# Kernel tuning notes

Hardware: AMD Instinct MI355X
Metric: run time of the kernel (lower is better)

Reference implementation:

```python
import jax, jax.numpy as jnp
import numpy as np

S, B, HID = 2048, 1, 2048
NH, HD = 16, 128  # heads, head_dim (kv_channels); NH*HD == HID
EPS = 1e-5


def setup_inputs() -> dict:
    key = jax.random.key(0)
    ks = jax.random.split(key, 5)
    sc_h = 1.0 / np.sqrt(HID)
    return {
        "hidden_states": jax.random.normal(ks[0], (S, B, HID), jnp.float32),
        "ln_weight": jnp.ones((HID,), jnp.float32),
        "ln_bias": jnp.zeros((HID,), jnp.float32),
        "qkv_weight": jax.random.normal(ks[1], (3 * HID, HID), jnp.float32) * sc_h,
        "qkv_bias": jax.random.normal(ks[2], (3 * HID,), jnp.float32) * 0.02,
        "proj_weight": jax.random.normal(ks[3], (HID, HID), jnp.float32) * sc_h,
        "proj_bias": jax.random.normal(ks[4], (HID,), jnp.float32) * 0.02,
    }


def reference(hidden_states, ln_weight, ln_bias, qkv_weight, qkv_bias, proj_weight, proj_bias):
    s, b, hid = hidden_states.shape
    # LayerNormLinear: LN over last dim, then fused QKV projection
    mu = jnp.mean(hidden_states, axis=-1, keepdims=True)
    var = jnp.mean(jnp.square(hidden_states - mu), axis=-1, keepdims=True)
    ln_x = (hidden_states - mu) * jax.lax.rsqrt(var + EPS) * ln_weight + ln_bias
    mixed = jnp.einsum('sbh,oh->sbo', ln_x, qkv_weight) + qkv_bias  # [S,B,3*HID]
    # fuse_qkv_params=False -> non-interleaved: reshape to [S,B,3*NH,HD], split on dim -2
    mixed = mixed.reshape(s, b, 3 * NH, HD)
    q, k, v = jnp.split(mixed, 3, axis=2)  # each [S,B,NH,HD]
    # scaled dot-product attention with causal mask
    scale = 1.0 / np.sqrt(HD)
    scores = jnp.einsum('sbhd,tbhd->bhst', q, k) * scale  # [B,NH,S,S]
    causal = jnp.tril(jnp.ones((s, s), bool))
    scores = jnp.where(causal, scores, -jnp.inf)
    probs = jax.nn.softmax(scores, axis=-1)
    ctx = jnp.einsum('bhst,tbhd->sbhd', probs, v).reshape(s, b, hid)
    # output projection
    out = jnp.einsum('sbh,oh->sbo', ctx, proj_weight) + proj_bias
    return out
```

## Files before the change

kernel.cpp:

```cpp
#include <hip/hip_runtime.h>
#include <stdint.h>

#define S_LEN 2048
#define HID   2048
#define NHEAD 16
#define HDIM  128
#define LDQK  4096

typedef unsigned short ushort_t;
using bf16x8 = __attribute__((ext_vector_type(8))) short;
using f32x4  = __attribute__((ext_vector_type(4))) float;

__device__ __forceinline__ float bf2f(ushort_t u) {
  union { uint32_t i; float f; } v; v.i = ((uint32_t)u) << 16; return v.f;
}
__device__ __forceinline__ ushort_t f2bf(float f) {
  union { float f; uint32_t i; } v; v.f = f;
  uint32_t r = v.i + 0x7fffu + ((v.i >> 16) & 1u);
  return (ushort_t)(r >> 16);
}
__device__ __forceinline__ void store_val(ushort_t* C, size_t idx, float v) { C[idx] = f2bf(v); }
__device__ __forceinline__ void store_val(float* C, size_t idx, float v) { C[idx] = v; }

__device__ __forceinline__ bf16x8 load8(const ushort_t* p) { return *(const bf16x8*)p; }
__device__ __forceinline__ bf16x8 load8(const float* p) {
  float4 a = *(const float4*)p, b = *(const float4*)(p + 4);
  ushort_t o[8] = { f2bf(a.x), f2bf(a.y), f2bf(a.z), f2bf(a.w),
                    f2bf(b.x), f2bf(b.y), f2bf(b.z), f2bf(b.w) };
  return *(const bf16x8*)o;
}

__device__ __forceinline__ void gl_lds16(const ushort_t* g, short* l) {
  __builtin_amdgcn_global_load_lds((const __attribute__((address_space(1))) void*)g,
                                   (__attribute__((address_space(3))) void*)l, 16, 0, 0);
}

__global__ __launch_bounds__(256) void cvt_f32_bf16_2(const float* __restrict__ s1,
                                                      ushort_t* __restrict__ d1, int n1,
                                                      const float* __restrict__ s2,
                                                      ushort_t* __restrict__ d2, int n2) {
  int i = blockIdx.x * 256 + threadIdx.x;
  const float* src; ushort_t* dst;
  if (i < n1) { src = s1; dst = d1; }
  else { i -= n1; if (i >= n2) return; src = s2; dst = d2; }
  float4 a = ((const float4*)src)[i * 2], b = ((const float4*)src)[i * 2 + 1];
  ushort_t o[8] = { f2bf(a.x), f2bf(a.y), f2bf(a.z), f2bf(a.w),
                    f2bf(b.x), f2bf(b.y), f2bf(b.z), f2bf(b.w) };
  ((uint4*)dst)[i] = *(const uint4*)o;
}

__global__ __launch_bounds__(256) void ln_kernel(const float* __restrict__ x,
                                                 const float* __restrict__ w,
                                                 const float* __restrict__ b,
                                                 ushort_t* __restrict__ y) {
  const int row = blockIdx.x;
  const int t = threadIdx.x;
  const float4* xr = (const float4*)(x + (size_t)row * HID);
  float4 v0 = xr[t], v1 = xr[t + 256];
  float s  = v0.x + v0.y + v0.z + v0.w + v1.x + v1.y + v1.z + v1.w;
  float ss = v0.x*v0.x + v0.y*v0.y + v0.z*v0.z + v0.w*v0.w
           + v1.x*v1.x + v1.y*v1.y + v1.z*v1.z + v1.w*v1.w;
#pragma unroll
  for (int off = 32; off > 0; off >>= 1) { s += __shfl_xor(s, off, 64); ss += __shfl_xor(ss, off, 64); }
  __shared__ float red[8];
  const int wv = t >> 6;
  if ((t & 63) == 0) { red[wv * 2] = s; red[wv * 2 + 1] = ss; }
  __syncthreads();
  s  = red[0] + red[2] + red[4] + red[6];
  ss = red[1] + red[3] + red[5] + red[7];
  const float mu   = s * (1.f / HID);
  const float var  = ss * (1.f / HID) - mu * mu;
  const float rstd = rsqrtf(var + 1e-5f);
  const float4* wr = (const float4*)w;
  const float4* br = (const float4*)b;
  float4 w0 = wr[t], w1 = wr[t + 256];
  float4 b0 = br[t], b1 = br[t + 256];
  ushort_t* yr = y + (size_t)row * HID;
  ushort_t o0[4] = { f2bf((v0.x - mu) * rstd * w0.x + b0.x), f2bf((v0.y - mu) * rstd * w0.y + b0.y),
                     f2bf((v0.z - mu) * rstd * w0.z + b0.z), f2bf((v0.w - mu) * rstd * w0.w + b0.w) };
  ushort_t o1[4] = { f2bf((v1.x - mu) * rstd * w1.x + b1.x), f2bf((v1.y - mu) * rstd * w1.y + b1.y),
                     f2bf((v1.z - mu) * rstd * w1.z + b1.z), f2bf((v1.w - mu) * rstd * w1.w + b1.w) };
  *(uint2*)(&yr[4 * t])         = *(const uint2*)o0;
  *(uint2*)(&yr[4 * (t + 256)]) = *(const uint2*)o1;
}

template <int MT, bool SPLIT, typename OUT_T>
__global__ __launch_bounds__(256, 3) void gemm_lds(const ushort_t* __restrict__ A,
                                                   const ushort_t* __restrict__ B,
                                                   const float* __restrict__ bias,
                                                   OUT_T* __restrict__ C,
                                                   ushort_t* __restrict__ VTg,
                                                   int M, int N, int K, int ldc) {
  constexpr int MI = MT / 32;
  __shared__ __align__(16) short As[2][MT * 32];
  __shared__ __align__(16) short Bs[2][128 * 32];
  const int mb = blockIdx.x * MT, nb = blockIdx.y * 128;
  const int t = threadIdx.x, wave = t >> 6, lane = t & 63;
  const int wm = (wave >> 1) * (MT / 2), wn = (wave & 1) * 64;
  const int lrow = lane & 15, quad = lane >> 4;
  const int srow = lane >> 2, scol = (lane & 3) * 8;
  const f32x4 vzero = {0.f, 0.f, 0.f, 0.f};

  f32x4 acc[MI][4];
#pragma unroll
  for (int i = 0; i < MI; i++)
#pragma unroll
    for (int j = 0; j < 4; j++) acc[i][j] = vzero;

  auto stage = [&](int k0, int buf) {
#pragma unroll
    for (int kb = 0; kb < MT / 64; kb++) {
      const int c = wave * (MT / 64) + kb;
      gl_lds16(&A[(size_t)(mb + c * 16 + srow) * K + k0 + scol], &As[buf][c * 512]);
    }
#pragma unroll
    for (int kb = 0; kb < 2; kb++) {
      const int c = wave * 2 + kb;
      gl_lds16(&B[(size_t)(nb + c * 16 + srow) * K + k0 + scol], &Bs[buf][c * 512]);
    }
  };

  stage(0, 0);
  int cur = 0;
  for (int k0 = 0; k0 < K; k0 += 32) {
    __syncthreads();
    if (k0 + 32 < K) stage(k0 + 32, cur ^ 1);
    bf16x8 af[MI], bfg[4];
#pragma unroll
    for (int mi = 0; mi < MI; mi++) af[mi] = *(const bf16x8*)(&As[cur][(wm + mi * 16 + lrow) * 32 + quad * 8]);
#pragma unroll
    for (int ni = 0; ni < 4; ni++) bfg[ni] = *(const bf16x8*)(&Bs[cur][(wn + ni * 16 + lrow) * 32 + quad * 8]);
#pragma unroll
    for (int mi = 0; mi < MI; mi++)
#pragma unroll
      for (int ni = 0; ni < 4; ni++)
        acc[mi][ni] = __builtin_amdgcn_mfma_f32_16x16x32_bf16(af[mi], bfg[ni], acc[mi][ni], 0, 0, 0);
    cur ^= 1;
  }

#pragma unroll
  for (int mi = 0; mi < MI; mi++)
#pragma unroll
    for (int ni = 0; ni < 4; ni++) {
      const int col = nb + wn + ni * 16 + lrow;
      const float bv = bias[col];
      const int row0 = mb + wm + mi * 16 + quad * 4;
      if (SPLIT && col >= 4096) {
        ushort_t o4[4];
#pragma unroll
        for (int r = 0; r < 4; r++) o4[r] = f2bf(acc[mi][ni][r] + bv);
        *(uint2*)(&VTg[(size_t)(col - 4096) * S_LEN + row0]) = *(const uint2*)o4;
      } else {
#pragma unroll
        for (int r = 0; r < 4; r++)
          store_val(C, (size_t)(row0 + r) * ldc + col, acc[mi][ni][r] + bv);
      }
    }
}

template <bool SPLIT, typename OUT_T, typename BT>
__global__ __launch_bounds__(256, 3) void gemm_bt(const ushort_t* __restrict__ A,
                                                  const BT* __restrict__ B,
                                                  const float* __restrict__ bias,
                                                  OUT_T* __restrict__ C,
                                                  ushort_t* __restrict__ VTg,
                                                  int M, int N, int K, int ldc) {
  __shared__ __align__(16) short As[128 * 40];
  __shared__ __align__(16) short Bs[128 * 40];
  const int mb = blockIdx.x * 128, nb = blockIdx.y * 128;
  const int t = threadIdx.x, wave = t >> 6, lane = t & 63;
  const int wm = (wave >> 1) * 64, wn = (wave & 1) * 64;
  const int lrow = lane & 15, quad = lane >> 4;
  const f32x4 vzero = {0.f, 0.f, 0.f, 0.f};
  f32x4 acc[4][4];
#pragma unroll
  for (int i = 0; i < 4; i++)
#pragma unroll
    for (int j = 0; j < 4; j++) acc[i][j] = vzero;
  for (int k0 = 0; k0 < K; k0 += 32) {
    __syncthreads();
#pragma unroll
    for (int i = 0; i < 2; i++) {
      int c = t + 256 * i;
      int r = c >> 2, kc = (c & 3) * 8;
      *(bf16x8*)(&As[r * 40 + kc]) = load8(&A[(size_t)(mb + r) * K + k0 + kc]);
      *(bf16x8*)(&Bs[r * 40 + kc]) = load8(&B[(size_t)(nb + r) * K + k0 + kc]);
    }
    __syncthreads();
    bf16x8 af[4], bfg[4];
#pragma unroll
    for (int mi = 0; mi < 4; mi++) af[mi] = *(const bf16x8*)(&As[(wm + mi * 16 + lrow) * 40 + quad * 8]);
#pragma unroll
    for (int ni = 0; ni < 4; ni++) bfg[ni] = *(const bf16x8*)(&Bs[(wn + ni * 16 + lrow) * 40 + quad * 8]);
#pragma unroll
    for (int mi = 0; mi < 4; mi++)
#pragma unroll
      for (int ni = 0; ni < 4; ni++)
        acc[mi][ni] = __builtin_amdgcn_mfma_f32_16x16x32_bf16(af[mi], bfg[ni], acc[mi][ni], 0, 0, 0);
  }
#pragma unroll
  for (int mi = 0; mi < 4; mi++)
#pragma unroll
    for (int ni = 0; ni < 4; ni++) {
      const int col = nb + wn + ni * 16 + lrow;
      const float bv = bias[col];
      const int row0 = mb + wm + mi * 16 + quad * 4;
      if (SPLIT && col >= 4096) {
        ushort_t o4[4];
#pragma unroll
        for (int r = 0; r < 4; r++) o4[r] = f2bf(acc[mi][ni][r] + bv);
        *(uint2*)(&VTg[(size_t)(col - 4096) * S_LEN + row0]) = *(const uint2*)o4;
      } else {
#pragma unroll
        for (int r = 0; r < 4; r++)
          store_val(C, (size_t)(row0 + r) * ldc + col, acc[mi][ni][r] + bv);
      }
    }
}

__global__ __launch_bounds__(256, 2) void attn_kernel(const ushort_t* __restrict__ mixedQK,
                                                      const ushort_t* __restrict__ vtg,
                                                      ushort_t* __restrict__ ctx) {
  const int b = blockIdx.x;
  const int h = b & 15;
  const int bi = b >> 4;
  const int qblk = (bi < 16) ? (31 - bi) : (bi - 16);
  const int t = threadIdx.x;
  const int wave = t >> 6, lane = t & 63;
  const int lrow = lane & 15, quad = lane >> 4;
  const float scale = 0.08838834764831845f;
  const float SHIFT = 8.0f;

  __shared__ __align__(16) short Ks[64 * 128];
  __shared__ __align__(16) short VTs[2][128 * 64];
  __shared__ __align__(16) short Ps[4][16 * 72];

  const int krow_off = wave * 4 + (lane >> 4);
  const int kgrp = (lane & 15) ^ krow_off;
  const int vrow_off = wave * 8 + (lane >> 3);
  const int vgrp = (lane & 7) ^ (lane >> 3);
  const ushort_t* Kbase = mixedQK + 2048 + h * HDIM;
  const ushort_t* Vbase = vtg + (size_t)h * HDIM * S_LEN;

  const f32x4 vzero = {0.f, 0.f, 0.f, 0.f};

  auto stageK = [&](int kv0) {
#pragma unroll
    for (int i = 0; i < 4; i++)
      gl_lds16(Kbase + (size_t)(kv0 + i * 16 + krow_off) * LDQK + kgrp * 8,
               &Ks[(i * 256 + wave * 64) * 8]);
  };
  auto stageV = [&](int kv0, int buf) {
#pragma unroll
    for (int i = 0; i < 4; i++)
      gl_lds16(Vbase + (size_t)(i * 32 + vrow_off) * S_LEN + kv0 + vgrp * 8,
               &VTs[buf][(i * 256 + wave * 64) * 8]);
  };

  stageK(0);
  stageV(0, 0);

  const int ntiles = qblk + 1;
  const int q0 = qblk * 64 + wave * 16;

  bf16x8 qf[4];
  {
    const ushort_t* Qb = mixedQK + (size_t)(q0 + lrow) * LDQK + h * HDIM;
#pragma unroll
    for (int c = 0; c < 4; c++) qf[c] = *(const bf16x8*)(Qb + c * 32 + quad * 8);
  }

  float lsum[4] = {0.f, 0.f, 0.f, 0.f};
  f32x4 acc[8];
#pragma unroll
  for (int d = 0; d < 8; d++) acc[d] = vzero;

  for (int tk = 0; tk < ntiles; ++tk) {
    const int kv0 = tk * 64;
    __syncthreads();
    if (tk + 1 < ntiles) stageV((tk + 1) * 64, (tk + 1) & 1);

    f32x4 sc[4];
#pragma unroll
    for (int ni = 0; ni < 4; ni++) sc[ni] = vzero;
    __builtin_amdgcn_s_setprio(1);
#pragma unroll
    for (int ni = 0; ni < 4; ni++)
#pragma unroll
      for (int c = 0; c < 4; c++) {
        bf16x8 kf = *(const bf16x8*)(&Ks[(((ni * 16 + lrow) << 4) + ((c * 4 + quad) ^ lrow)) * 8]);
        sc[ni] = __builtin_amdgcn_mfma_f32_16x16x32_bf16(qf[c], kf, sc[ni], 0, 0, 0);
      }
    __builtin_amdgcn_s_setprio(0);

    asm volatile("s_waitcnt lgkmcnt(0)\n\ts_barrier" ::: "memory");
    if (tk + 1 < ntiles) stageK((tk + 1) * 64);

    short* P = &Ps[wave][0];
#pragma unroll
    for (int r = 0; r < 4; r++) {
      const int row = q0 + quad * 4 + r;
#pragma unroll
      for (int ni = 0; ni < 4; ni++) {
        const int col = kv0 + ni * 16 + lrow;
        float pe = (col > row) ? 0.f : __expf(sc[ni][r] * scale - SHIFT);
        lsum[r] += pe;
        P[(quad * 4 + r) * 72 + ni * 16 + lrow] = (short)f2bf(pe);
      }
    }

    bf16x8 pf[2];
#pragma unroll
    for (int c = 0; c < 2; c++) pf[c] = *(const bf16x8*)(&P[lrow * 72 + c * 32 + quad * 8]);

    const short* Vc = VTs[tk & 1];
    __builtin_amdgcn_s_setprio(1);
#pragma unroll
    for (int d = 0; d < 8; d++)
#pragma unroll
      for (int c = 0; c < 2; c++) {
        bf16x8 vf = *(const bf16x8*)(&Vc[(((d * 16 + lrow) << 3) + ((c * 4 + quad) ^ (lrow & 7))) * 8]);
        acc[d] = __builtin_amdgcn_mfma_f32_16x16x32_bf16(pf[c], vf, acc[d], 0, 0, 0);
      }
    __builtin_amdgcn_s_setprio(0);
  }

  float inv_l[4];
#pragma unroll
  for (int r = 0; r < 4; r++) {
    float l = lsum[r];
#pragma unroll
    for (int off = 1; off < 16; off <<= 1) l += __shfl_xor(l, off, 16);
    inv_l[r] = 1.f / l;
  }
#pragma unroll
  for (int d = 0; d < 8; d++)
#pragma unroll
    for (int r = 0; r < 4; r++) {
      const int row = q0 + quad * 4 + r;
      ctx[(size_t)row * HID + h * HDIM + d * 16 + lrow] = f2bf(acc[d][r] * inv_l[r]);
    }
}

extern "C" void kernel_launch(void* const* d_in, const int* in_sizes, int n_in,
                              void* d_out, int out_size, void* d_ws, size_t ws_size,
                              hipStream_t stream) {
  const float* hidden = (const float*)d_in[0];
  const float* lnw    = (const float*)d_in[1];
  const float* lnb    = (const float*)d_in[2];
  const float* qkvw   = (const float*)d_in[3];
  const float* qkvb   = (const float*)d_in[4];
  const float* projw  = (const float*)d_in[5];
  const float* projb  = (const float*)d_in[6];
  float* out = (float*)d_out;

  char* ws = (char*)d_ws;
  ushort_t* ln_x    = (ushort_t*)ws;
  ushort_t* mixedQK = (ushort_t*)(ws + ((size_t)8 << 20));
  ushort_t* vtg     = (ushort_t*)(ws + ((size_t)24 << 20));
  ushort_t* qkvw_bf = (ushort_t*)(ws + ((size_t)32 << 20));
  ushort_t* projw_bf= (ushort_t*)(ws + ((size_t)56 << 20));
  ushort_t* ctxb    = ln_x;
  const bool big = ws_size >= ((size_t)64 << 20);

  ln_kernel<<<S_LEN, 256, 0, stream>>>(hidden, lnw, lnb, ln_x);
  if (big) {
    cvt_f32_bf16_2<<<8192, 256, 0, stream>>>(qkvw, qkvw_bf, 3 * HID * HID / 8,
                                             projw, projw_bf, HID * HID / 8);
    gemm_lds<128, true, ushort_t><<<dim3(16, 48), 256, 0, stream>>>(
        ln_x, qkvw_bf, qkvb, mixedQK, vtg, S_LEN, 3 * HID, HID, LDQK);
  } else {
    gemm_bt<true, ushort_t, float><<<dim3(16, 48), 256, 0, stream>>>(
        ln_x, qkvw, qkvb, mixedQK, vtg, S_LEN, 3 * HID, HID, LDQK);
  }
  attn_kernel<<<512, 256, 0, stream>>>(mixedQK, vtg, ctxb);
  if (big) {
    gemm_lds<64, false, float><<<dim3(32, 16), 256, 0, stream>>>(
        ctxb, projw_bf, projb, out, nullptr, S_LEN, HID, HID, HID);
  } else {
    gemm_bt<false, float, float><<<dim3(16, 16), 256, 0, stream>>>(
        ctxb, projw, projb, out, nullptr, S_LEN, HID, HID, HID);
  }
}
```

Baseline: 268.6 us.

## Replace QKV GEMM with 256x256-tile 8-wave ping-pong kernel

Adds a new GEMM kernel for the QKV projection that uses 256x256 output tiles, 8 waves per block, a 4-deep LDS ring with direct global-to-LDS loads, and XOR-swizzled LDS addressing. It splits each K-step into two MFMA phases separated by barriers, raises wave priority around the MFMA blocks, and remaps block IDs in an XCD-aware order. The larger tile increases data reuse per block and cuts global traffic, but gives only 192 blocks, which may underfill the GPU. It also uses more registers and LDS per block.

```diff
diff --git a/kernel.cpp b/kernel.cpp
--- a/kernel.cpp
+++ b/kernel.cpp
@@ -84,6 +84,120 @@
   *(uint2*)(&yr[4 * (t + 256)]) = *(const uint2*)o1;
 }
 
+template <bool SPLIT, typename OUT_T>
+__global__ __launch_bounds__(512, 2) void gemm_8p(const ushort_t* __restrict__ A,
+                                                  const ushort_t* __restrict__ B,
+                                                  const float* __restrict__ bias,
+                                                  OUT_T* __restrict__ C,
+                                                  ushort_t* __restrict__ VTg,
+                                                  int M, int N, int K, int ldc) {
+  __shared__ __align__(16) short As[4][256 * 32];
+  __shared__ __align__(16) short Bs[4][256 * 32];
+
+  const int nwg = gridDim.x, cpx = nwg >> 3;
+  const int bid = blockIdx.x;
+  const int swz = (bid & 7) * cpx + (bid >> 3);
+  const int rowsb = M >> 8;
+  const int mb = (swz % rowsb) * 256, nb = (swz / rowsb) * 256;
+
+  const int t = threadIdx.x, wave = t >> 6, lane = t & 63;
+  const int wm = wave >> 2, wn = wave & 3;
+  const int lrow = lane & 15, quad = lane >> 4;
+  const int NE = K >> 5;
+
+  const int srow4 = lane >> 2;
+  const int ssl = ((lane & 3) ^ ((lane >> 3) & 3)) * 8;
+  const int xs = (quad ^ ((lrow >> 1) & 3)) * 8;
+
+  const f32x4 vzero = {0.f, 0.f, 0.f, 0.f};
+  f32x4 acc[8][4];
+#pragma unroll
+  for (int i = 0; i < 8; i++)
+#pragma unroll
+    for (int j = 0; j < 4; j++) acc[i][j] = vzero;
+
+  auto stageH = [&](const ushort_t* Mat, int rowbase, int colbase, short* ldsbase) {
+#pragma unroll
+    for (int i = 0; i < 2; i++) {
+      const int r0 = i * 128 + wave * 16;
+      gl_lds16(&Mat[(size_t)(rowbase + r0 + srow4) * K + colbase + ssl],
+               ldsbase + r0 * 32);
+    }
+  };
+
+  stageH(A, mb, 0,  As[0]);
+  stageH(B, nb, 0,  Bs[0]);
+  stageH(A, mb, 32, As[1]);
+  stageH(B, nb, 32, Bs[1]);
+  asm volatile("s_waitcnt vmcnt(4)" ::: "memory");
+  __builtin_amdgcn_s_barrier();
+
+  for (int e = 0; e < NE; ++e) {
+    const short* Ab = As[e & 3];
+    const short* Bb = Bs[e & 3];
+    const int cnext = (e + 2) * 32;
+    const bool more = (e + 2 < NE);
+
+    bf16x8 bfr[4], afr[4];
+#pragma unroll
+    for (int ni = 0; ni < 4; ni++)
+      bfr[ni] = *(const bf16x8*)(&Bb[(wn * 64 + ni * 16 + lrow) * 32 + xs]);
+#pragma unroll
+    for (int mi = 0; mi < 4; mi++)
+      afr[mi] = *(const bf16x8*)(&Ab[(wm * 128 + mi * 16 + lrow) * 32 + xs]);
+    if (more) stageH(A, mb, cnext, As[(e + 2) & 3]);
+
+    __builtin_amdgcn_s_barrier();
+    asm volatile("s_waitcnt lgkmcnt(0)" ::: "memory");
+    __builtin_amdgcn_s_setprio(1);
+#pragma unroll
+    for (int mi = 0; mi < 4; mi++)
+#pragma unroll
+      for (int ni = 0; ni < 4; ni++)
+        acc[mi][ni] = __builtin_amdgcn_mfma_f32_16x16x32_bf16(afr[mi], bfr[ni], acc[mi][ni], 0, 0, 0);
+    __builtin_amdgcn_s_setprio(0);
+    __builtin_amdgcn_s_barrier();
+
+    bf16x8 af2[4];
+#pragma unroll
+    for (int mi = 0; mi < 4; mi++)
+      af2[mi] = *(const bf16x8*)(&Ab[(wm * 128 + (mi + 4) * 16 + lrow) * 32 + xs]);
+    if (more) stageH(B, nb, cnext, Bs[(e + 2) & 3]);
+
+    if (more) asm volatile("s_waitcnt vmcnt(4)" ::: "memory");
+    else      asm volatile("s_waitcnt vmcnt(0)" ::: "memory");
+    __builtin_amdgcn_s_barrier();
+    asm volatile("s_waitcnt lgkmcnt(0)" ::: "memory");
+    __builtin_amdgcn_s_setprio(1);
+#pragma unroll
+    for (int mi = 0; mi < 4; mi++)
+#pragma unroll
+      for (int ni = 0; ni < 4; ni++)
+        acc[mi + 4][ni] = __builtin_amdgcn_mfma_f32_16x16x32_bf16(af2[mi], bfr[ni], acc[mi + 4][ni], 0, 0, 0);
+    __builtin_amdgcn_s_setprio(0);
+    __builtin_amdgcn_s_barrier();
+  }
+
+#pragma unroll
+  for (int mi = 0; mi < 8; mi++)
+#pragma unroll
+    for (int ni = 0; ni < 4; ni++) {
+      const int col = nb + wn * 64 + ni * 16 + lrow;
+      const float bv = bias[col];
+      const int row0 = mb + wm * 128 + mi * 16 + quad * 4;
+      if (SPLIT && col >= 4096) {
+        ushort_t o4[4];
+#pragma unroll
+        for (int r = 0; r < 4; r++) o4[r] = f2bf(acc[mi][ni][r] + bv);
+        *(uint2*)(&VTg[(size_t)(col - 4096) * S_LEN + row0]) = *(const uint2*)o4;
+      } else {
+#pragma unroll
+        for (int r = 0; r < 4; r++)
+          store_val(C, (size_t)(row0 + r) * ldc + col, acc[mi][ni][r] + bv);
+      }
+    }
+}
+
 template <int MT, bool SPLIT, typename OUT_T>
 __global__ __launch_bounds__(256, 3) void gemm_lds(const ushort_t* __restrict__ A,
                                                    const ushort_t* __restrict__ B,
@@ -367,7 +481,7 @@
   if (big) {
     cvt_f32_bf16_2<<<8192, 256, 0, stream>>>(qkvw, qkvw_bf, 3 * HID * HID / 8,
                                              projw, projw_bf, HID * HID / 8);
-    gemm_lds<128, true, ushort_t><<<dim3(16, 48), 256, 0, stream>>>(
+    gemm_8p<true, ushort_t><<<192, 512, 0, stream>>>(
         ln_x, qkvw_bf, qkvb, mixedQK, vtg, S_LEN, 3 * HID, HID, LDQK);
   } else {
     gemm_bt<true, ushort_t, float><<<dim3(16, 48), 256, 0, stream>>>(
```

Result: no change. 271.4 us (+1.0%).
